# Optimization experiments

Hardware: AMD Instinct MI355X
Metric: run time of the kernel (lower is better)

## Reference

```python
import jax, jax.numpy as jnp
import numpy as np

N_NODES = 50000
N_EDGES = 800000
LN_EPS = 1e-5


def _segment_softmax_aggr(msg, t, dst, n):
    # SoftmaxAggregation(learn=True): alpha = softmax(msg * t) per dest segment, out = sum(alpha * msg)
    logits = msg * t  # [E, C]
    m = jax.ops.segment_max(logits, dst, num_segments=n)
    m = jnp.where(jnp.isfinite(m), m, 0.0)  # empty segments -> 0 to keep exp finite
    e = jnp.exp(logits - m[dst])
    denom = jax.ops.segment_sum(e, dst, num_segments=n)
    alpha = e / jnp.maximum(denom[dst], 1e-16)
    return jax.ops.segment_sum(alpha * msg, dst, num_segments=n)


def _sage_conv(x, src, dst, wp, bp, t, wl, bl, wr):
    # project=True: messages come from relu(lin(x)); root term uses ORIGINAL x
    xp = jax.nn.relu(x @ wp + bp)
    msg = xp[src]                                   # [E, C] gather
    aggr = _segment_softmax_aggr(msg, t, dst, x.shape[0])
    out = aggr @ wl + bl + x @ wr
    # normalize=True: L2 normalize rows (eps as in F.normalize)
    nrm = jnp.maximum(jnp.linalg.norm(out, axis=-1, keepdims=True), 1e-12)
    return out / nrm


def _mem_pool(x, k, w_conv, wl, bl):
    # PyG MemPooling, tau=1: Student-t kernel 1/(1+d^2)
    H, K, F = k.shape
    kk = k.reshape(H * K, F)
    d2 = (jnp.sum(kk * kk, -1)[:, None] + jnp.sum(x * x, -1)[None, :]
          - 2.0 * kk @ x.T)                          # [H*K, N]
    d2 = jnp.maximum(d2, 0.0)
    dist = 1.0 / (1.0 + d2)
    dist = dist.reshape(H, K, -1).transpose(0, 2, 1)  # [H, N, K]
    S = dist / jnp.sum(dist, -1, keepdims=True)       # per-head normalize over clusters
    S = jnp.einsum('h,hnk->nk', w_conv, S)            # 1x1 conv mixing heads (no bias)
    S = jax.nn.softmax(S, axis=-1)                    # [N, K]
    xp = S.T @ x                                      # [K, F]
    return xp @ wl + bl                               # [K, out]


def setup_inputs() -> dict:
    key = jax.random.key(0)
    ks = jax.random.split(key, 20)
    rn = lambda i, shp, s: jax.random.normal(ks[i], shp, dtype=jnp.float32) * s
    inp = {
        'x': rn(0, (N_NODES, 64), 1.0),
        'edge_index': jax.random.randint(ks[1], (2, N_EDGES), 0, N_NODES, dtype=jnp.int32),
        'w_proj1': rn(2, (64, 64), 0.1), 'b_proj1': rn(3, (64,), 0.05),
        't1': jnp.ones((64,), jnp.float32),
        'w_l1': rn(4, (64, 256), 0.1), 'b_l1': rn(5, (256,), 0.05),
        'w_r1': rn(6, (64, 256), 0.1),
        'w_proj2': rn(7, (256, 256), 0.05), 'b_proj2': rn(8, (256,), 0.05),
        't2': jnp.ones((256,), jnp.float32),
        'w_l2': rn(9, (256, 128), 0.05), 'b_l2': rn(10, (128,), 0.05),
        'w_r2': rn(11, (256, 128), 0.05),
        'k_mem': rn(12, (4, 4, 128), 1.0),
        'w_conv': rn(13, (4,), 0.5),
        'w_memlin': rn(14, (128, 128), 0.08), 'b_memlin': rn(15, (128,), 0.05),
        'w_fx': rn(16, (128, 64), 0.08), 'b_fx': rn(17, (64,), 0.05),
        'gamma': jnp.ones((64,), jnp.float32),
        'beta': jnp.zeros((64,), jnp.float32),
    }
    return inp


def reference(x, edge_index, w_proj1, b_proj1, t1, w_l1, b_l1, w_r1,
              w_proj2, b_proj2, t2, w_l2, b_l2, w_r2,
              k_mem, w_conv, w_memlin, b_memlin, w_fx, b_fx, gamma, beta):
    src, dst = edge_index[0], edge_index[1]
    h = _sage_conv(x, src, dst, w_proj1, b_proj1, t1, w_l1, b_l1, w_r1)
    h = jax.nn.relu(h)                              # dropout = identity (eval)
    h = _sage_conv(h, src, dst, w_proj2, b_proj2, t2, w_l2, b_l2, w_r2)
    h = jax.nn.relu(h)
    pooled = _mem_pool(h, k_mem, w_conv, w_memlin, b_memlin)  # [4, 128]
    g = jnp.mean(pooled, axis=0, keepdims=True)     # global_mean_pool -> [1, 128]
    y = g @ w_fx + b_fx                             # [1, 64]
    mu = jnp.mean(y, -1, keepdims=True)
    var = jnp.var(y, -1, keepdims=True)
    y = (y - mu) / jnp.sqrt(var + LN_EPS) * gamma + beta
    return jax.nn.relu(y)
```

## Files before the change

kernel.cpp:

```cpp
#include <hip/hip_runtime.h>
#include <hip/hip_bf16.h>

#define N_NODES 50000
#define N_EDGES 800000
#define NB 196
#define PC_SLICES 2048

typedef __attribute__((ext_vector_type(8))) short short8;
typedef __attribute__((ext_vector_type(4))) float f32x4;
typedef __attribute__((ext_vector_type(2))) float f32x2;

#define QSCALE2 (2.f / 255.f)
#define QINV2   127.5f
#define QSCALE1 (12.75f / 255.f)
#define QINV1   20.f

__device__ __forceinline__ float us2f(unsigned short u) {
    return __uint_as_float(((unsigned int)u) << 16);
}
__device__ __forceinline__ unsigned short f2bu(float f) {
    unsigned int u = __float_as_uint(f);
    unsigned int r = (u + 0x7fffu + ((u >> 16) & 1u)) >> 16;
    return (unsigned short)r;
}
__device__ __forceinline__ float exp2_hw(float x) {
    float r;
    __asm__("v_exp_f32 %0, %1" : "=v"(r) : "v"(x));
    return r;
}
__device__ __forceinline__ void async16(const void* g, void* l) {
    __builtin_amdgcn_global_load_lds(
        (const __attribute__((address_space(1))) unsigned int*)g,
        (__attribute__((address_space(3))) unsigned int*)l, 16, 0, 0);
}
#define LOG2E 1.44269504088896f

__global__ void k_hist(const int* __restrict__ dst, int* __restrict__ counts) {
    int e = blockIdx.x * 256 + threadIdx.x;
    if (e < N_EDGES) atomicAdd(&counts[dst[e]], 1);
}

__global__ __launch_bounds__(256) void k_scan1(const int* __restrict__ counts,
                                               int* __restrict__ row_ptr,
                                               int* __restrict__ partial) {
    __shared__ int sd[256];
    int t = threadIdx.x, i = blockIdx.x * 256 + t;
    int v = (i < N_NODES) ? counts[i] : 0;
    sd[t] = v;
    __syncthreads();
    for (int off = 1; off < 256; off <<= 1) {
        int o = (t >= off) ? sd[t - off] : 0;
        __syncthreads();
        sd[t] += o;
        __syncthreads();
    }
    if (i < N_NODES) row_ptr[i] = sd[t] - v;
    if (t == 255) partial[blockIdx.x] = sd[255];
}

__global__ __launch_bounds__(256) void k_scan3b(int* __restrict__ row_ptr,
                                                const int* __restrict__ partial,
                                                int* __restrict__ cursor) {
    __shared__ int sd[256];
    int t = threadIdx.x;
    sd[t] = (t < blockIdx.x) ? partial[t] : 0;
    __syncthreads();
    for (int off = 128; off > 0; off >>= 1) {
        if (t < off) sd[t] += sd[t + off];
        __syncthreads();
    }
    int base = sd[0];
    int i = blockIdx.x * 256 + t;
    if (i < N_NODES) {
        int v = row_ptr[i] + base;
        row_ptr[i] = v;
        cursor[i] = v;
    }
    if (blockIdx.x == 0 && t == 0) row_ptr[N_NODES] = N_EDGES;
}

__global__ void k_scatter(const int* __restrict__ src, const int* __restrict__ dst,
                          int* __restrict__ cursor, int* __restrict__ src_sorted) {
    int e = blockIdx.x * 256 + threadIdx.x;
    if (e < N_EDGES) {
        int d = dst[e];
        int pos = atomicAdd(&cursor[d], 1);
        src_sorted[pos] = src[e];
    }
}

__global__ __launch_bounds__(256) void k_dhist(const int* __restrict__ counts,
                                               int* __restrict__ bcnt) {
    __shared__ int h[64];
    int t = threadIdx.x;
    if (t < 64) h[t] = 0;
    __syncthreads();
    int i = blockIdx.x * 256 + t;
    if (i < N_NODES) {
        int d = counts[i];
        d = d > 63 ? 63 : d;
        atomicAdd(&h[d], 1);
    }
    __syncthreads();
    if (t < 64) bcnt[blockIdx.x * 64 + t] = h[t];
}

__global__ __launch_bounds__(256) void k_dscan2(const int* __restrict__ bcnt,
                                                int* __restrict__ boff,
                                                int* __restrict__ dtot) {
    __shared__ int sd[256];
    int d = blockIdx.x, t = threadIdx.x;
    int v = (t < NB) ? bcnt[t * 64 + d] : 0;
    sd[t] = v;
    __syncthreads();
    for (int off = 1; off < 256; off <<= 1) {
        int o = (t >= off) ? sd[t - off] : 0;
        __syncthreads();
        sd[t] += o;
        __syncthreads();
    }
    if (t < NB) boff[t * 64 + d] = sd[t] - v;
    if (t == 255) dtot[d] = sd[255];
}

__global__ __launch_bounds__(256) void k_dscatter(const int* __restrict__ counts,
                                                  const int* __restrict__ boff,
                                                  const int* __restrict__ dtot,
                                                  int* __restrict__ perm) {
    __shared__ int h[64];
    __shared__ int dbaseS[64];
    int t = threadIdx.x;
    if (t < 64) {
        h[t] = 0;
        int v = dtot[t];
        int s = v;
        for (int off = 1; off < 64; off <<= 1) {
            int o = __shfl_up(s, off);
            if (t >= off) s += o;
        }
        dbaseS[t] = s - v;
    }
    __syncthreads();
    int i = blockIdx.x * 256 + t;
    if (i < N_NODES) {
        int d = counts[i];
        d = d > 63 ? 63 : d;
        int rank = atomicAdd(&h[d], 1);
        perm[dbaseS[d] + boff[blockIdx.x * 64 + d] + rank] = i;
    }
}

#define XCAST_N (N_NODES * 64)
__global__ __launch_bounds__(256) void k_prep(const float* __restrict__ x,
                                              const float* __restrict__ wp1,
                                              const float* __restrict__ wl1,
                                              const float* __restrict__ wr1,
                                              const float* __restrict__ wp2,
                                              const float* __restrict__ wl2,
                                              const float* __restrict__ wr2,
                                              unsigned short* __restrict__ cat1,
                                              unsigned short* __restrict__ B0T,
                                              unsigned short* __restrict__ B1T,
                                              unsigned short* __restrict__ BP2T,
                                              unsigned short* __restrict__ B2T) {
    int idx = blockIdx.x * 256 + threadIdx.x;
    if (idx < XCAST_N) {
        int i = idx >> 6, j = idx & 63;
        cat1[i * 128 + 64 + j] = f2bu(x[idx]);
        return;
    }
    int w = idx - XCAST_N;
    if (w < 4096)  { int k = w >> 6, n = w & 63;  B0T[n * 64 + k] = f2bu(wp1[w]); return; }
    w -= 4096;
    if (w < 16384) { int k = w >> 8, n = w & 255; B1T[n * 128 + k] = f2bu(wl1[w]); return; }
    w -= 16384;
    if (w < 16384) { int k = w >> 8, n = w & 255; B1T[n * 128 + 64 + k] = f2bu(wr1[w]); return; }
    w -= 16384;
    if (w < 65536) { int k = w >> 8, n = w & 255; BP2T[n * 256 + k] = f2bu(wp2[w]); return; }
    w -= 65536;
    if (w < 32768) { int k = w >> 7, n = w & 127; B2T[n * 512 + k] = f2bu(wl2[w]); return; }
    w -= 32768;
    if (w < 32768) { int k = w >> 7, n = w & 127; B2T[n * 512 + 256 + k] = f2bu(wr2[w]); return; }
}

template<int K, int C, int LDA, int LDOUT, int OUT_OFF, int EP, int WPB, int MH>
__global__ __launch_bounds__(256, WPB) void k_gemm(const unsigned short* __restrict__ A,
                                                   const unsigned short* __restrict__ BT,
                                                   const float* __restrict__ bias,
                                                   void* __restrict__ outv,
                                                   const float* __restrict__ kmem,
                                                   const float* __restrict__ wconv,
                                                   float* __restrict__ Sm,
                                                   float qinv) {
    constexpr int NT = C / 16;
    constexpr int SAE = 64 * MH * 64;
    constexpr int SBE = C * 64;
    constexpr int STAGE_B = (SAE + SBE) * 2;
    constexpr int RPLD = (EP == 2) ? (C + 4) : ((EP == 3) ? (C + 16) : (C + 8));
    constexpr int RP_B = 64 * RPLD * (EP == 2 ? 4 : (EP == 3 ? 1 : 2));
    constexpr int SMEM_B = STAGE_B > RP_B ? STAGE_B : RP_B;
    constexpr int POOL_B = (EP == 2) ? (2048 * 4 + 64 + 16) : 16;
    __shared__ __align__(16) char smem[SMEM_B + POOL_B];
    unsigned short* sA = (unsigned short*)smem;
    unsigned short* sB = sA + SAE;
    float* kls  = (float*)(smem + SMEM_B);
    float* kk2s = kls + 2048;
    float* wcs  = kk2s + 16;

    int t = threadIdx.x;
    int wid = t >> 6, lane = t & 63;
    int lrow = lane & 15, quad = lane >> 4;
    int m0 = blockIdx.x * (64 * MH);

    if (EP == 2) {
        for (int i = t; i < 2048; i += 256) kls[i] = kmem[i];
        if (t < 4) wcs[t] = wconv[t];
        __syncthreads();
        if (t < 16) {
            float s = 0.f;
            for (int f = 0; f < 128; ++f) { float v = kls[t * 128 + f]; s += v * v; }
            kk2s[t] = s;
        }
    }

    f32x4 acc[MH][NT];
#pragma unroll
    for (int h = 0; h < MH; ++h)
#pragma unroll
        for (int nt = 0; nt < NT; ++nt)
#pragma unroll
            for (int r = 0; r < 4; ++r) acc[h][nt][r] = 0.f;

    for (int k0 = 0; k0 < K; k0 += 64) {
        __syncthreads();
        for (int i = t; i < 64 * MH * 8; i += 256) {
            int r = i >> 3, seg = i & 7;
            size_t m = (size_t)(m0 + r);
            async16(&A[m * LDA + k0 + ((seg ^ (r & 7)) << 3)],
                    (char*)sA + (size_t)(i - lane) * 16);
        }
        for (int i = t; i < C * 8; i += 256) {
            int n = i >> 3, seg = i & 7;
            async16(&BT[(size_t)n * K + k0 + ((seg ^ (n & 7)) << 3)],
                    (char*)sB + (size_t)(i - lane) * 16);
        }
        __syncthreads();
#pragma unroll
        for (int kk = 0; kk < 2; ++kk) {
            int sw = lrow & 7;
            short8 av[MH];
#pragma unroll
            for (int h = 0; h < MH; ++h)
                av[h] = *(const short8*)&sA[(h * 64 + wid * 16 + lrow) * 64 +
                                            (((kk * 4 + quad) ^ sw) << 3)];
#pragma unroll
            for (int nt = 0; nt < NT; ++nt) {
                short8 bfg = *(const short8*)&sB[(nt * 16 + lrow) * 64 +
                                                 (((kk * 4 + quad) ^ sw) << 3)];
#pragma unroll
                for (int h = 0; h < MH; ++h)
                    acc[h][nt] = __builtin_amdgcn_mfma_f32_16x16x32_bf16(av[h], bfg, acc[h][nt], 0, 0, 0);
            }
        }
    }

#pragma unroll
    for (int h = 0; h < MH; ++h) {
#pragma unroll
        for (int nt = 0; nt < NT; ++nt) {
            float bv = bias[nt * 16 + lrow];
#pragma unroll
            for (int r = 0; r < 4; ++r) acc[h][nt][r] += bv;
        }
        if (EP == 1 || EP == 2) {
#pragma unroll
            for (int r = 0; r < 4; ++r) {
                float ss = 0.f;
#pragma unroll
                for (int nt = 0; nt < NT; ++nt) ss += acc[h][nt][r] * acc[h][nt][r];
                ss += __shfl_xor(ss, 1);
                ss += __shfl_xor(ss, 2);
                ss += __shfl_xor(ss, 4);
                ss += __shfl_xor(ss, 8);
                float rinv = 1.f / fmaxf(sqrtf(ss), 1e-12f);
#pragma unroll
                for (int nt = 0; nt < NT; ++nt)
                    acc[h][nt][r] = fmaxf(acc[h][nt][r] * rinv, 0.f);
            }
        } else {
#pragma unroll
            for (int nt = 0; nt < NT; ++nt)
#pragma unroll
                for (int r = 0; r < 4; ++r) acc[h][nt][r] = fmaxf(acc[h][nt][r], 0.f);
        }
    }

    __syncthreads();
#pragma unroll
    for (int h = 0; h < MH; ++h) {
        if (EP == 2) {
            float* rp = (float*)smem;
#pragma unroll
            for (int nt = 0; nt < NT; ++nt)
#pragma unroll
                for (int r = 0; r < 4; ++r)
                    rp[(wid * 16 + quad * 4 + r) * RPLD + nt * 16 + lrow] = acc[h][nt][r];
            __syncthreads();
            float* outp = (float*)outv;
            for (int i = t; i < 64 * C / 4; i += 256) {
                int f = i * 4, r = f / C, c = f % C;
                int m = m0 + h * 64 + r;
                if (m < N_NODES)
                    *(float4*)&outp[(size_t)m * LDOUT + OUT_OFF + c] = *(const float4*)&rp[r * RPLD + c];
            }
            {
                int row = t >> 2, p = t & 3;
                int cbase = p * 32;
                float dots[16];
#pragma unroll
                for (int k = 0; k < 16; ++k) dots[k] = 0.f;
                float x2 = 0.f;
#pragma unroll
                for (int j = 0; j < 8; ++j) {
                    int c4 = (j + p * 2) & 7;
                    float4 xv = *(const float4*)&rp[row * RPLD + cbase + c4 * 4];
                    x2 += xv.x * xv.x + xv.y * xv.y + xv.z * xv.z + xv.w * xv.w;
#pragma unroll
                    for (int k = 0; k < 16; ++k) {
                        float4 kv = *(const float4*)&kls[k * 128 + cbase + c4 * 4];
                        dots[k] += xv.x * kv.x + xv.y * kv.y + xv.z * kv.z + xv.w * kv.w;
                    }
                }
#pragma unroll
                for (int k = 0; k < 16; ++k) {
                    dots[k] += __shfl_xor(dots[k], 1);
                    dots[k] += __shfl_xor(dots[k], 2);
                }
                x2 += __shfl_xor(x2, 1);
                x2 += __shfl_xor(x2, 2);
                if (p == 0) {
                    int m = m0 + h * 64 + row;
                    if (m < N_NODES) {
                        float dist[16];
#pragma unroll
                        for (int k = 0; k < 16; ++k) {
                            float d2 = fmaxf(kk2s[k] + x2 - 2.f * dots[k], 0.f);
                            dist[k] = 1.f / (1.f + d2);
                        }
                        float s0 = 0.f, s1 = 0.f, s2 = 0.f, s3 = 0.f;
#pragma unroll
                        for (int hh = 0; hh < 4; ++hh) {
                            float den = dist[hh * 4] + dist[hh * 4 + 1] +
                                        dist[hh * 4 + 2] + dist[hh * 4 + 3];
                            float inv = wcs[hh] / den;
                            s0 += dist[hh * 4 + 0] * inv;
                            s1 += dist[hh * 4 + 1] * inv;
                            s2 += dist[hh * 4 + 2] * inv;
                            s3 += dist[hh * 4 + 3] * inv;
                        }
                        float mx = fmaxf(fmaxf(s0, s1), fmaxf(s2, s3));
                        float e0 = __expf(s0 - mx), e1 = __expf(s1 - mx);
                        float e2 = __expf(s2 - mx), e3 = __expf(s3 - mx);
                        float inv = 1.f / (e0 + e1 + e2 + e3);
                        *(float4*)&Sm[(size_t)m * 4] =
                            make_float4(e0 * inv, e1 * inv, e2 * inv, e3 * inv);
                    }
                }
            }
            __syncthreads();
        } else if (EP == 3) {
            unsigned char* rp = (unsigned char*)smem;
#pragma unroll
            for (int nt = 0; nt < NT; ++nt)
#pragma unroll
                for (int r = 0; r < 4; ++r) {
                    float q = fminf(__builtin_rintf(acc[h][nt][r] * qinv), 255.f);
                    rp[(wid * 16 + quad * 4 + r) * RPLD + nt * 16 + lrow] = (unsigned char)(int)q;
                }
            __syncthreads();
            unsigned char* outp = (unsigned char*)outv;
            for (int i = t; i < 64 * C / 16; i += 256) {
                int f = i * 16, r = f / C, c = f % C;
                int m = m0 + h * 64 + r;
                if (m < N_NODES)
                    *(uint4*)&outp[(size_t)m * LDOUT + OUT_OFF + c] = *(const uint4*)&rp[r * RPLD + c];
            }
            __syncthreads();
        } else {
            unsigned short* rp = (unsigned short*)smem;
#pragma unroll
            for (int nt = 0; nt < NT; ++nt)
#pragma unroll
                for (int r = 0; r < 4; ++r)
                    rp[(wid * 16 + quad * 4 + r) * RPLD + nt * 16 + lrow] = f2bu(acc[h][nt][r]);
            __syncthreads();
            unsigned short* outp = (unsigned short*)outv;
            for (int i = t; i < 64 * C / 8; i += 256) {
                int f = i * 8, r = f / C, c = f % C;
                int m = m0 + h * 64 + r;
                if (m < N_NODES)
                    *(uint4*)&outp[(size_t)m * LDOUT + OUT_OFF + c] = *(const uint4*)&rp[r * RPLD + c];
            }
            __syncthreads();
        }
    }
}

__global__ __launch_bounds__(128) void k_aggr256(const unsigned char* __restrict__ xp,
                                                 const float* __restrict__ tvec,
                                                 const int* __restrict__ row_ptr,
                                                 const int* __restrict__ srcs,
                                                 const int* __restrict__ perm,
                                                 unsigned short* __restrict__ outp) {
    int t = threadIdx.x & 63;
    int wid = threadIdx.x >> 6;
    int n = __builtin_amdgcn_readfirstlane(perm[blockIdx.x * 2 + wid]);
    float4 tv4 = *(const float4*)&tvec[t * 4];
    f32x2 tv01 = {tv4.x * (LOG2E * QSCALE2), tv4.y * (LOG2E * QSCALE2)};
    f32x2 tv23 = {tv4.z * (LOG2E * QSCALE2), tv4.w * (LOG2E * QSCALE2)};
    int beg = __builtin_amdgcn_readfirstlane(row_ptr[n]);
    int end = __builtin_amdgcn_readfirstlane(row_ptr[n + 1]);
    f32x2 se01 = {0.f, 0.f}, se23 = {0.f, 0.f};
    f32x2 sem01 = {0.f, 0.f}, sem23 = {0.f, 0.f};
    int e = beg;
#define EDGE_BODY(VV, MSK)                                                     \
    {                                                                          \
        f32x2 m01 = {(float)((VV) & 0xFFu), (float)(((VV) >> 8) & 0xFFu)};     \
        f32x2 m23 = {(float)(((VV) >> 16) & 0xFFu), (float)((VV) >> 24)};      \
        f32x2 l01 = m01 * tv01, l23 = m23 * tv23;                              \
        f32x2 w01, w23;                                                        \
        w01.x = exp2_hw(l01.x) * (MSK); w01.y = exp2_hw(l01.y) * (MSK);        \
        w23.x = exp2_hw(l23.x) * (MSK); w23.y = exp2_hw(l23.y) * (MSK);        \
        se01 += w01; se23 += w23;                                              \
        sem01 = __builtin_elementwise_fma(w01, m01, sem01);                    \
        sem23 = __builtin_elementwise_fma(w23, m23, sem23);                    \
    }
    for (; e + 16 <= end; e += 16) {
        unsigned int v[16];
#pragma unroll
        for (int j = 0; j < 16; ++j) {
            const unsigned char* p = xp + (size_t)srcs[e + j] * 256;
            v[j] = *(const unsigned int*)&p[t * 4];
        }
#pragma unroll
        for (int j = 0; j < 16; ++j) EDGE_BODY(v[j], 1.f)
    }
    for (; e + 8 <= end; e += 8) {
        unsigned int v[8];
#pragma unroll
        for (int j = 0; j < 8; ++j) {
            const unsigned char* p = xp + (size_t)srcs[e + j] * 256;
            v[j] = *(const unsigned int*)&p[t * 4];
        }
#pragma unroll
        for (int j = 0; j < 8; ++j) EDGE_BODY(v[j], 1.f)
    }
    if (e < end) {
        int last = end - 1;
        unsigned int v[8];
#pragma unroll
        for (int j = 0; j < 8; ++j) {
            int ee = e + j;
            ee = ee < end ? ee : last;
            const unsigned char* p = xp + (size_t)srcs[ee] * 256;
            v[j] = *(const unsigned int*)&p[t * 4];
        }
#pragma unroll
        for (int j = 0; j < 8; ++j) {
            float msk = (e + j < end) ? 1.f : 0.f;
            EDGE_BODY(v[j], msk)
        }
    }
#undef EDGE_BODY
    ushort4 o;
    o.x = f2bu(QSCALE2 * sem01.x / fmaxf(se01.x, 1e-16f));
    o.y = f2bu(QSCALE2 * sem01.y / fmaxf(se01.y, 1e-16f));
    o.z = f2bu(QSCALE2 * sem23.x / fmaxf(se23.x, 1e-16f));
    o.w = f2bu(QSCALE2 * sem23.y / fmaxf(se23.y, 1e-16f));
    *(ushort4*)&outp[(size_t)n * 512 + t * 4] = o;
}

__global__ __launch_bounds__(128) void k_aggr64(const unsigned char* __restrict__ xp,
                                                const float* __restrict__ tvec,
                                                const int* __restrict__ row_ptr,
                                                const int* __restrict__ srcs,
                                                const int* __restrict__ perm,
                                                unsigned short* __restrict__ outp) {
    int c = threadIdx.x & 63;
    int wid = threadIdx.x >> 6;
    int n = __builtin_amdgcn_readfirstlane(perm[blockIdx.x * 2 + wid]);
    float tv = tvec[c] * (LOG2E * QSCALE1);
    int beg = __builtin_amdgcn_readfirstlane(row_ptr[n]);
    int end = __builtin_amdgcn_readfirstlane(row_ptr[n + 1]);
    float se = 0.f, sem = 0.f;
    int e = beg;
    for (; e + 16 <= end; e += 16) {
        unsigned char v[16];
#pragma unroll
        for (int j = 0; j < 16; ++j)
            v[j] = xp[(size_t)srcs[e + j] * 64 + c];
#pragma unroll
        for (int j = 0; j < 16; ++j) {
            float msg = (float)v[j];
            float w = exp2_hw(msg * tv);
            se += w;
            sem = fmaf(w, msg, sem);
        }
    }
    for (; e + 8 <= end; e += 8) {
        unsigned char v[8];
#pragma unroll
        for (int j = 0; j < 8; ++j)
            v[j] = xp[(size_t)srcs[e + j] * 64 + c];
#pragma unroll
        for (int j = 0; j < 8; ++j) {
            float msg = (float)v[j];
            float w = exp2_hw(msg * tv);
            se += w;
            sem = fmaf(w, msg, sem);
        }
    }
    if (e < end) {
        int last = end - 1;
        unsigned char v[8];
#pragma unroll
        for (int j = 0; j < 8; ++j) {
            int ee = e + j;
            ee = ee < end ? ee : last;
            v[j] = xp[(size_t)srcs[ee] * 64 + c];
        }
#pragma unroll
        for (int j = 0; j < 8; ++j) {
            float msk = (e + j < end) ? 1.f : 0.f;
            float msg = (float)v[j];
            float w = exp2_hw(msg * tv) * msk;
            se += w;
            sem = fmaf(w, msg, sem);
        }
    }
    outp[(size_t)n * 128 + c] = f2bu(QSCALE1 * sem / fmaxf(se, 1e-16f));
}

__global__ __launch_bounds__(256) void k_pool_c(const float* __restrict__ h2,
                                                const float* __restrict__ Sm,
                                                float* __restrict__ part) {
    int t = threadIdx.x;
    int c = t & 127, sub = t >> 7;
    int slice = blockIdx.x * 2 + sub;
    float a0 = 0.f, a1 = 0.f, a2 = 0.f, a3 = 0.f;
    for (int n = slice; n < N_NODES; n += PC_SLICES) {
        float xv = h2[(size_t)n * 128 + c];
        float4 sv = *(const float4*)&Sm[(size_t)n * 4];
        a0 = fmaf(sv.x, xv, a0);
        a1 = fmaf(sv.y, xv, a1);
        a2 = fmaf(sv.z, xv, a2);
        a3 = fmaf(sv.w, xv, a3);
    }
    float* p = &part[(size_t)slice * 512];
    p[0 * 128 + c] = a0;
    p[1 * 128 + c] = a1;
    p[2 * 128 + c] = a2;
    p[3 * 128 + c] = a3;
}

__global__ __launch_bounds__(256) void k_pool_b(const float* __restrict__ part,
                                                float* __restrict__ pooled) {
    int j = blockIdx.x;
    float s = 0.f;
    for (int b = threadIdx.x; b < PC_SLICES; b += 256) s += part[(size_t)b * 512 + j];
#pragma unroll
    for (int off = 32; off > 0; off >>= 1) s += __shfl_xor(s, off);
    __shared__ float red[4];
    int lane = threadIdx.x & 63, wid = threadIdx.x >> 6;
    if (lane == 0) red[wid] = s;
    __syncthreads();
    if (threadIdx.x == 0) pooled[j] = red[0] + red[1] + red[2] + red[3];
}

__global__ __launch_bounds__(128) void k_final(const float* __restrict__ pooled,
                                               const float* __restrict__ wmem,
                                               const float* __restrict__ bmem,
                                               const float* __restrict__ wfx,
                                               const float* __restrict__ bfx,
                                               const float* __restrict__ gamma,
                                               const float* __restrict__ beta,
                                               float* __restrict__ out) {
    __shared__ float gx[128], g[128];
    int t = threadIdx.x;
    gx[t] = 0.25f * (pooled[t] + pooled[128 + t] + pooled[256 + t] + pooled[384 + t]);
    __syncthreads();
    float acc = bmem[t];
    for (int f = 0; f < 128; ++f) acc = fmaf(gx[f], wmem[f * 128 + t], acc);
    g[t] = acc;
    __syncthreads();
    if (t < 64) {
        float y = bfx[t];
        for (int f = 0; f < 128; ++f) y = fmaf(g[f], wfx[f * 64 + t], y);
        float s = y, s2 = y * y;
#pragma unroll
        for (int off = 32; off > 0; off >>= 1) {
            s += __shfl_xor(s, off);
            s2 += __shfl_xor(s2, off);
        }
        float mu = s * (1.f / 64.f);
        float var = s2 * (1.f / 64.f) - mu * mu;
        float v = (y - mu) / sqrtf(var + 1e-5f) * gamma[t] + beta[t];
        out[t] = fmaxf(v, 0.f);
    }
}

extern "C" void kernel_launch(void* const* d_in, const int* in_sizes, int n_in,
                              void* d_out, int out_size, void* d_ws, size_t ws_size,
                              hipStream_t stream) {
    const float* x        = (const float*)d_in[0];
    const int*   ei       = (const int*)  d_in[1];
    const float* w_proj1  = (const float*)d_in[2];
    const float* b_proj1  = (const float*)d_in[3];
    const float* t1       = (const float*)d_in[4];
    const float* w_l1     = (const float*)d_in[5];
    const float* b_l1     = (const float*)d_in[6];
    const float* w_r1     = (const float*)d_in[7];
    const float* w_proj2  = (const float*)d_in[8];
    const float* b_proj2  = (const float*)d_in[9];
    const float* t2       = (const float*)d_in[10];
    const float* w_l2     = (const float*)d_in[11];
    const float* b_l2     = (const float*)d_in[12];
    const float* w_r2     = (const float*)d_in[13];
    const float* k_mem    = (const float*)d_in[14];
    const float* w_conv   = (const float*)d_in[15];
    const float* w_memlin = (const float*)d_in[16];
    const float* b_memlin = (const float*)d_in[17];
    const float* w_fx     = (const float*)d_in[18];
    const float* b_fx     = (const float*)d_in[19];
    const float* gamma    = (const float*)d_in[20];
    const float* beta     = (const float*)d_in[21];
    const int* src = ei;
    const int* dst = ei + N_EDGES;
    (void)in_sizes; (void)n_in; (void)out_size; (void)ws_size;

    char* W = (char*)d_ws;
    const size_t MB = 1024 * 1024;
    int*   row_ptr    = (int*)(W + 0);
    int*   cursor     = (int*)(W + 256 * 1024);
    int*   partial    = (int*)(W + 512 * 1024);
    int*   dtot       = (int*)(W + 512 * 1024 + 4096);
    int*   bcnt       = (int*)(W + 520 * 1024);
    int*   boff       = (int*)(W + 576 * 1024);
    int*   src_sorted = (int*)(W + 768 * 1024);
    unsigned short* cat1 = (unsigned short*)(W + 4 * MB);
    unsigned char*  xp1  = (unsigned char*)(W + 17 * MB);
    unsigned short* cat2 = (unsigned short*)(W + 24 * MB);
    unsigned char*  xp2  = (unsigned char*)(W + 76 * MB);
    float* h2     = (float*)(W + 102 * MB);
    float* Sm     = (float*)(W + 128 * MB);
    float* pooled = (float*)(W + 131 * MB);
    unsigned short* B0T  = (unsigned short*)(W + 133 * MB);
    unsigned short* B1T  = (unsigned short*)(W + 134 * MB);
    unsigned short* BP2T = (unsigned short*)(W + 135 * MB);
    unsigned short* B2T  = (unsigned short*)(W + 136 * MB);
    int*   perm   = (int*)(W + 138 * MB);
    float* part   = (float*)(W + 140 * MB);

    hipMemsetAsync(cursor, 0, N_NODES * sizeof(int), stream);
    k_hist<<<(N_EDGES + 255) / 256, 256, 0, stream>>>(dst, cursor);
    k_dhist<<<NB, 256, 0, stream>>>(cursor, bcnt);
    k_scan1<<<NB, 256, 0, stream>>>(cursor, row_ptr, partial);
    k_dscan2<<<64, 256, 0, stream>>>(bcnt, boff, dtot);
    k_dscatter<<<NB, 256, 0, stream>>>(cursor, boff, dtot, perm);
    k_scan3b<<<NB, 256, 0, stream>>>(row_ptr, partial, cursor);
    k_scatter<<<(N_EDGES + 255) / 256, 256, 0, stream>>>(src, dst, cursor, src_sorted);

    k_prep<<<(XCAST_N + 167936 + 255) / 256, 256, 0, stream>>>(
        x, w_proj1, w_l1, w_r1, w_proj2, w_l2, w_r2, cat1, B0T, B1T, BP2T, B2T);

    const int GB = (N_NODES + 127) / 128;
    const int AGB = N_NODES / 2;

    k_gemm<64, 64, 128, 64, 0, 3, 4, 2><<<GB, 256, 0, stream>>>(
        cat1 + 64, B0T, b_proj1, xp1, nullptr, nullptr, nullptr, QINV1);
    k_aggr64<<<AGB, 128, 0, stream>>>(xp1, t1, row_ptr, src_sorted, perm, cat1);
    k_gemm<128, 256, 128, 512, 256, 1, 3, 2><<<GB, 256, 0, stream>>>(
        cat1, B1T, b_l1, cat2, nullptr, nullptr, nullptr, 0.f);

    k_gemm<256, 256, 512, 256, 0, 3, 3, 2><<<GB, 256, 0, stream>>>(
        cat2 + 256, BP2T, b_proj2, xp2, nullptr, nullptr, nullptr, QINV2);
    k_aggr256<<<AGB, 128, 0, stream>>>(xp2, t2, row_ptr, src_sorted, perm, cat2);
    k_gemm<512, 128, 512, 128, 0, 2, 3, 2><<<GB, 256, 0, stream>>>(
        cat2, B2T, b_l2, h2, k_mem, w_conv, Sm, 0.f);

    k_pool_c<<<PC_SLICES / 2, 256, 0, stream>>>(h2, Sm, part);
    k_pool_b<<<512, 256, 0, stream>>>(part, pooled);
    k_final<<<1, 128, 0, stream>>>(pooled, w_memlin, b_memlin, w_fx, b_fx, gamma, beta,
                                   (float*)d_out);
}
```

Baseline: 377.0 us.

## Double-buffer aggregation gathers, reverse degree order, vectorize prep casts

New measurement: 387.0 us. 2.6% more time.

```diff
diff --git a/kernel.cpp b/kernel.cpp
--- a/kernel.cpp
+++ b/kernel.cpp
@@ -151,6 +151,7 @@
 }
 
 #define XCAST_N (N_NODES * 64)
+#define PREP_TOT (XCAST_N + 167936)
 __global__ __launch_bounds__(256) void k_prep(const float* __restrict__ x,
                                               const float* __restrict__ wp1,
                                               const float* __restrict__ wl1,
@@ -163,24 +164,38 @@
                                               unsigned short* __restrict__ B1T,
                                               unsigned short* __restrict__ BP2T,
                                               unsigned short* __restrict__ B2T) {
-    int idx = blockIdx.x * 256 + threadIdx.x;
+    int idx = (blockIdx.x * 256 + threadIdx.x) * 4;
     if (idx < XCAST_N) {
         int i = idx >> 6, j = idx & 63;
-        cat1[i * 128 + 64 + j] = f2bu(x[idx]);
+        float4 v = *(const float4*)&x[idx];
+        ushort4 o = { f2bu(v.x), f2bu(v.y), f2bu(v.z), f2bu(v.w) };
+        *(ushort4*)&cat1[i * 128 + 64 + j] = o;
         return;
     }
     int w = idx - XCAST_N;
-    if (w < 4096)  { int k = w >> 6, n = w & 63;  B0T[n * 64 + k] = f2bu(wp1[w]); return; }
+    if (w < 4096)  { float4 v = *(const float4*)&wp1[w]; int k = w >> 6, n = w & 63;
+                     B0T[n*64+k]=f2bu(v.x); B0T[(n+1)*64+k]=f2bu(v.y);
+                     B0T[(n+2)*64+k]=f2bu(v.z); B0T[(n+3)*64+k]=f2bu(v.w); return; }
     w -= 4096;
-    if (w < 16384) { int k = w >> 8, n = w & 255; B1T[n * 128 + k] = f2bu(wl1[w]); return; }
+    if (w < 16384) { float4 v = *(const float4*)&wl1[w]; int k = w >> 8, n = w & 255;
+                     B1T[n*128+k]=f2bu(v.x); B1T[(n+1)*128+k]=f2bu(v.y);
+                     B1T[(n+2)*128+k]=f2bu(v.z); B1T[(n+3)*128+k]=f2bu(v.w); return; }
     w -= 16384;
-    if (w < 16384) { int k = w >> 8, n = w & 255; B1T[n * 128 + 64 + k] = f2bu(wr1[w]); return; }
+    if (w < 16384) { float4 v = *(const float4*)&wr1[w]; int k = w >> 8, n = w & 255;
+                     B1T[n*128+64+k]=f2bu(v.x); B1T[(n+1)*128+64+k]=f2bu(v.y);
+                     B1T[(n+2)*128+64+k]=f2bu(v.z); B1T[(n+3)*128+64+k]=f2bu(v.w); return; }
     w -= 16384;
-    if (w < 65536) { int k = w >> 8, n = w & 255; BP2T[n * 256 + k] = f2bu(wp2[w]); return; }
+    if (w < 65536) { float4 v = *(const float4*)&wp2[w]; int k = w >> 8, n = w & 255;
+                     BP2T[n*256+k]=f2bu(v.x); BP2T[(n+1)*256+k]=f2bu(v.y);
+                     BP2T[(n+2)*256+k]=f2bu(v.z); BP2T[(n+3)*256+k]=f2bu(v.w); return; }
     w -= 65536;
-    if (w < 32768) { int k = w >> 7, n = w & 127; B2T[n * 512 + k] = f2bu(wl2[w]); return; }
+    if (w < 32768) { float4 v = *(const float4*)&wl2[w]; int k = w >> 7, n = w & 127;
+                     B2T[n*512+k]=f2bu(v.x); B2T[(n+1)*512+k]=f2bu(v.y);
+                     B2T[(n+2)*512+k]=f2bu(v.z); B2T[(n+3)*512+k]=f2bu(v.w); return; }
     w -= 32768;
-    if (w < 32768) { int k = w >> 7, n = w & 127; B2T[n * 512 + 256 + k] = f2bu(wr2[w]); return; }
+    if (w < 32768) { float4 v = *(const float4*)&wr2[w]; int k = w >> 7, n = w & 127;
+                     B2T[n*512+256+k]=f2bu(v.x); B2T[(n+1)*512+256+k]=f2bu(v.y);
+                     B2T[(n+2)*512+256+k]=f2bu(v.z); B2T[(n+3)*512+256+k]=f2bu(v.w); return; }
 }
 
 template<int K, int C, int LDA, int LDOUT, int OUT_OFF, int EP, int WPB, int MH>
@@ -414,7 +429,7 @@
                                                  unsigned short* __restrict__ outp) {
     int t = threadIdx.x & 63;
     int wid = threadIdx.x >> 6;
-    int n = __builtin_amdgcn_readfirstlane(perm[blockIdx.x * 2 + wid]);
+    int n = __builtin_amdgcn_readfirstlane(perm[(N_NODES / 2 - 1 - blockIdx.x) * 2 + wid]);
     float4 tv4 = *(const float4*)&tvec[t * 4];
     f32x2 tv01 = {tv4.x * (LOG2E * QSCALE2), tv4.y * (LOG2E * QSCALE2)};
     f32x2 tv23 = {tv4.z * (LOG2E * QSCALE2), tv4.w * (LOG2E * QSCALE2)};
@@ -422,56 +437,68 @@
     int end = __builtin_amdgcn_readfirstlane(row_ptr[n + 1]);
     f32x2 se01 = {0.f, 0.f}, se23 = {0.f, 0.f};
     f32x2 sem01 = {0.f, 0.f}, sem23 = {0.f, 0.f};
-    int e = beg;
-#define EDGE_BODY(VV, MSK)                                                     \
+
+#define EDGE_BODY(VV)                                                          \
     {                                                                          \
         f32x2 m01 = {(float)((VV) & 0xFFu), (float)(((VV) >> 8) & 0xFFu)};     \
         f32x2 m23 = {(float)(((VV) >> 16) & 0xFFu), (float)((VV) >> 24)};      \
         f32x2 l01 = m01 * tv01, l23 = m23 * tv23;                              \
         f32x2 w01, w23;                                                        \
-        w01.x = exp2_hw(l01.x) * (MSK); w01.y = exp2_hw(l01.y) * (MSK);        \
-        w23.x = exp2_hw(l23.x) * (MSK); w23.y = exp2_hw(l23.y) * (MSK);        \
+        w01.x = exp2_hw(l01.x); w01.y = exp2_hw(l01.y);                        \
+        w23.x = exp2_hw(l23.x); w23.y = exp2_hw(l23.y);                        \
         se01 += w01; se23 += w23;                                              \
         sem01 = __builtin_elementwise_fma(w01, m01, sem01);                    \
         sem23 = __builtin_elementwise_fma(w23, m23, sem23);                    \
     }
-    for (; e + 16 <= end; e += 16) {
-        unsigned int v[16];
-#pragma unroll
-        for (int j = 0; j < 16; ++j) {
-            const unsigned char* p = xp + (size_t)srcs[e + j] * 256;
-            v[j] = *(const unsigned int*)&p[t * 4];
-        }
-#pragma unroll
-        for (int j = 0; j < 16; ++j) EDGE_BODY(v[j], 1.f)
-    }
-    for (; e + 8 <= end; e += 8) {
-        unsigned int v[8];
-#pragma unroll
-        for (int j = 0; j < 8; ++j) {
-            const unsigned char* p = xp + (size_t)srcs[e + j] * 256;
-            v[j] = *(const unsigned int*)&p[t * 4];
-        }
-#pragma unroll
-        for (int j = 0; j < 8; ++j) EDGE_BODY(v[j], 1.f)
-    }
-    if (e < end) {
-        int last = end - 1;
-        unsigned int v[8];
-#pragma unroll
-        for (int j = 0; j < 8; ++j) {
-            int ee = e + j;
-            ee = ee < end ? ee : last;
-            const unsigned char* p = xp + (size_t)srcs[ee] * 256;
-            v[j] = *(const unsigned int*)&p[t * 4];
-        }
-#pragma unroll
-        for (int j = 0; j < 8; ++j) {
-            float msk = (e + j < end) ? 1.f : 0.f;
-            EDGE_BODY(v[j], msk)
+#define LOAD16C(V, E)                                                          \
+    _Pragma("unroll")                                                          \
+    for (int j = 0; j < 16; ++j) {                                             \
+        int ee = (E) + j; ee = ee < end ? ee : end - 1;                        \
+        const unsigned char* p = xp + (size_t)srcs[ee] * 256;                  \
+        V[j] = *(const unsigned int*)&p[t * 4];                                \
+    }
+#define BODY16U(V)                                                             \
+    _Pragma("unroll") for (int j = 0; j < 16; ++j) EDGE_BODY(V[j])
+#define TAIL16(V)                                                              \
+    do {                                                                       \
+        if (end - e == 16) { BODY16U(V) }                                      \
+        else {                                                                 \
+            _Pragma("unroll")                                                  \
+            for (int j = 0; j < 16; ++j) {                                     \
+                unsigned int vv = (e + j < end) ? V[j] : 0u;                   \
+                EDGE_BODY(vv)                                                  \
+            }                                                                  \
+            float ninv = (float)(16 - (end - e));                              \
+            se01.x -= ninv; se01.y -= ninv; se23.x -= ninv; se23.y -= ninv;    \
+        }                                                                      \
+    } while (0)
+
+    unsigned int vA[16], vB[16];
+    int e = beg;
+    int nb = (end - beg + 15) >> 4;
+    if (nb > 0) {
+        LOAD16C(vA, e)
+        int b = 0;
+        while (b + 2 < nb) {
+            LOAD16C(vB, e + 16)
+            BODY16U(vA)
+            LOAD16C(vA, e + 32)
+            BODY16U(vB)
+            e += 32; b += 2;
+        }
+        if (b + 2 == nb) {
+            LOAD16C(vB, e + 16)
+            BODY16U(vA)
+            e += 16;
+            TAIL16(vB);
+        } else {
+            TAIL16(vA);
         }
     }
 #undef EDGE_BODY
+#undef LOAD16C
+#undef BODY16U
+#undef TAIL16
     ushort4 o;
     o.x = f2bu(QSCALE2 * sem01.x / fmaxf(se01.x, 1e-16f));
     o.y = f2bu(QSCALE2 * sem01.y / fmaxf(se01.y, 1e-16f));
@@ -488,56 +515,66 @@
                                                 unsigned short* __restrict__ outp) {
     int c = threadIdx.x & 63;
     int wid = threadIdx.x >> 6;
-    int n = __builtin_amdgcn_readfirstlane(perm[blockIdx.x * 2 + wid]);
+    int n = __builtin_amdgcn_readfirstlane(perm[(N_NODES / 2 - 1 - blockIdx.x) * 2 + wid]);
     float tv = tvec[c] * (LOG2E * QSCALE1);
     int beg = __builtin_amdgcn_readfirstlane(row_ptr[n]);
     int end = __builtin_amdgcn_readfirstlane(row_ptr[n + 1]);
     float se = 0.f, sem = 0.f;
+
+#define EDGE_BODY1(VV)                                                         \
+    {                                                                          \
+        float msg = (float)(VV);                                               \
+        float w = exp2_hw(msg * tv);                                           \
+        se += w;                                                               \
+        sem = fmaf(w, msg, sem);                                               \
+    }
+#define LOAD16C1(V, E)                                                         \
+    _Pragma("unroll")                                                          \
+    for (int j = 0; j < 16; ++j) {                                             \
+        int ee = (E) + j; ee = ee < end ? ee : end - 1;                        \
+        V[j] = xp[(size_t)srcs[ee] * 64 + c];                                  \
+    }
+#define BODY16U1(V)                                                            \
+    _Pragma("unroll") for (int j = 0; j < 16; ++j) EDGE_BODY1(V[j])
+#define TAIL161(V)                                                             \
+    do {                                                                       \
+        if (end - e == 16) { BODY16U1(V) }                                     \
+        else {                                                                 \
+            _Pragma("unroll")                                                  \
+            for (int j = 0; j < 16; ++j) {                                     \
+                unsigned int vv = (e + j < end) ? (unsigned int)V[j] : 0u;     \
+                EDGE_BODY1(vv)                                                 \
+            }                                                                  \
+            se -= (float)(16 - (end - e));                                     \
+        }                                                                      \
+    } while (0)
+
+    unsigned char vA[16], vB[16];
     int e = beg;
-    for (; e + 16 <= end; e += 16) {
-        unsigned char v[16];
-#pragma unroll
-        for (int j = 0; j < 16; ++j)
-            v[j] = xp[(size_t)srcs[e + j] * 64 + c];
-#pragma unroll
-        for (int j = 0; j < 16; ++j) {
-            float msg = (float)v[j];
-            float w = exp2_hw(msg * tv);
-            se += w;
-            sem = fmaf(w, msg, sem);
-        }
-    }
-    for (; e + 8 <= end; e += 8) {
-        unsigned char v[8];
-#pragma unroll
-        for (int j = 0; j < 8; ++j)
-            v[j] = xp[(size_t)srcs[e + j] * 64 + c];
-#pragma unroll
-        for (int j = 0; j < 8; ++j) {
-            float msg = (float)v[j];
-            float w = exp2_hw(msg * tv);
-            se += w;
-            sem = fmaf(w, msg, sem);
-        }
-    }
-    if (e < end) {
-        int last = end - 1;
-        unsigned char v[8];
-#pragma unroll
-        for (int j = 0; j < 8; ++j) {
-            int ee = e + j;
-            ee = ee < end ? ee : last;
-            v[j] = xp[(size_t)srcs[ee] * 64 + c];
-        }
-#pragma unroll
-        for (int j = 0; j < 8; ++j) {
-            float msk = (e + j < end) ? 1.f : 0.f;
-            float msg = (float)v[j];
-            float w = exp2_hw(msg * tv) * msk;
-            se += w;
-            sem = fmaf(w, msg, sem);
-        }
-    }
+    int nb = (end - beg + 15) >> 4;
+    if (nb > 0) {
+        LOAD16C1(vA, e)
+        int b = 0;
+        while (b + 2 < nb) {
+            LOAD16C1(vB, e + 16)
+            BODY16U1(vA)
+            LOAD16C1(vA, e + 32)
+            BODY16U1(vB)
+            e += 32; b += 2;
+        }
+        if (b + 2 == nb) {
+            LOAD16C1(vB, e + 16)
+            BODY16U1(vA)
+            e += 16;
+            TAIL161(vB);
+        } else {
+            TAIL161(vA);
+        }
+    }
+#undef EDGE_BODY1
+#undef LOAD16C1
+#undef BODY16U1
+#undef TAIL161
     outp[(size_t)n * 128 + c] = f2bu(QSCALE1 * sem / fmaxf(se, 1e-16f));
 }
 
@@ -670,7 +707,7 @@
     k_scan3b<<<NB, 256, 0, stream>>>(row_ptr, partial, cursor);
     k_scatter<<<(N_EDGES + 255) / 256, 256, 0, stream>>>(src, dst, cursor, src_sorted);
 
-    k_prep<<<(XCAST_N + 167936 + 255) / 256, 256, 0, stream>>>(
+    k_prep<<<(PREP_TOT / 4 + 255) / 256, 256, 0, stream>>>(
         x, w_proj1, w_l1, w_r1, w_proj2, w_l2, w_r2, cat1, B0T, B1T, BP2T, B2T);
 
     const int GB = (N_NODES + 127) / 128;
```

## Use persistent grid-stride aggregation kernels and vectorize the prep cast

Applied to the files above, without the earlier changes.

Measured after the change: 374.0 us. Within noise of the previous version (-0.8%).

```diff
diff --git a/kernel.cpp b/kernel.cpp
--- a/kernel.cpp
+++ b/kernel.cpp
@@ -5,6 +5,7 @@
 #define N_EDGES 800000
 #define NB 196
 #define PC_SLICES 2048
+#define AGG_GRID 2048
 
 typedef __attribute__((ext_vector_type(8))) short short8;
 typedef __attribute__((ext_vector_type(4))) float f32x4;
@@ -151,6 +152,7 @@
 }
 
 #define XCAST_N (N_NODES * 64)
+#define PREP_TOT (XCAST_N + 167936)
 __global__ __launch_bounds__(256) void k_prep(const float* __restrict__ x,
                                               const float* __restrict__ wp1,
                                               const float* __restrict__ wl1,
@@ -163,24 +165,38 @@
                                               unsigned short* __restrict__ B1T,
                                               unsigned short* __restrict__ BP2T,
                                               unsigned short* __restrict__ B2T) {
-    int idx = blockIdx.x * 256 + threadIdx.x;
+    int idx = (blockIdx.x * 256 + threadIdx.x) * 4;
     if (idx < XCAST_N) {
         int i = idx >> 6, j = idx & 63;
-        cat1[i * 128 + 64 + j] = f2bu(x[idx]);
+        float4 v = *(const float4*)&x[idx];
+        ushort4 o = { f2bu(v.x), f2bu(v.y), f2bu(v.z), f2bu(v.w) };
+        *(ushort4*)&cat1[i * 128 + 64 + j] = o;
         return;
     }
     int w = idx - XCAST_N;
-    if (w < 4096)  { int k = w >> 6, n = w & 63;  B0T[n * 64 + k] = f2bu(wp1[w]); return; }
+    if (w < 4096)  { float4 v = *(const float4*)&wp1[w]; int k = w >> 6, n = w & 63;
+                     B0T[n*64+k]=f2bu(v.x); B0T[(n+1)*64+k]=f2bu(v.y);
+                     B0T[(n+2)*64+k]=f2bu(v.z); B0T[(n+3)*64+k]=f2bu(v.w); return; }
     w -= 4096;
-    if (w < 16384) { int k = w >> 8, n = w & 255; B1T[n * 128 + k] = f2bu(wl1[w]); return; }
+    if (w < 16384) { float4 v = *(const float4*)&wl1[w]; int k = w >> 8, n = w & 255;
+                     B1T[n*128+k]=f2bu(v.x); B1T[(n+1)*128+k]=f2bu(v.y);
+                     B1T[(n+2)*128+k]=f2bu(v.z); B1T[(n+3)*128+k]=f2bu(v.w); return; }
     w -= 16384;
-    if (w < 16384) { int k = w >> 8, n = w & 255; B1T[n * 128 + 64 + k] = f2bu(wr1[w]); return; }
+    if (w < 16384) { float4 v = *(const float4*)&wr1[w]; int k = w >> 8, n = w & 255;
+                     B1T[n*128+64+k]=f2bu(v.x); B1T[(n+1)*128+64+k]=f2bu(v.y);
+                     B1T[(n+2)*128+64+k]=f2bu(v.z); B1T[(n+3)*128+64+k]=f2bu(v.w); return; }
     w -= 16384;
-    if (w < 65536) { int k = w >> 8, n = w & 255; BP2T[n * 256 + k] = f2bu(wp2[w]); return; }
+    if (w < 65536) { float4 v = *(const float4*)&wp2[w]; int k = w >> 8, n = w & 255;
+                     BP2T[n*256+k]=f2bu(v.x); BP2T[(n+1)*256+k]=f2bu(v.y);
+                     BP2T[(n+2)*256+k]=f2bu(v.z); BP2T[(n+3)*256+k]=f2bu(v.w); return; }
     w -= 65536;
-    if (w < 32768) { int k = w >> 7, n = w & 127; B2T[n * 512 + k] = f2bu(wl2[w]); return; }
+    if (w < 32768) { float4 v = *(const float4*)&wl2[w]; int k = w >> 7, n = w & 127;
+                     B2T[n*512+k]=f2bu(v.x); B2T[(n+1)*512+k]=f2bu(v.y);
+                     B2T[(n+2)*512+k]=f2bu(v.z); B2T[(n+3)*512+k]=f2bu(v.w); return; }
     w -= 32768;
-    if (w < 32768) { int k = w >> 7, n = w & 127; B2T[n * 512 + 256 + k] = f2bu(wr2[w]); return; }
+    if (w < 32768) { float4 v = *(const float4*)&wr2[w]; int k = w >> 7, n = w & 127;
+                     B2T[n*512+256+k]=f2bu(v.x); B2T[(n+1)*512+256+k]=f2bu(v.y);
+                     B2T[(n+2)*512+256+k]=f2bu(v.z); B2T[(n+3)*512+256+k]=f2bu(v.w); return; }
 }
 
 template<int K, int C, int LDA, int LDOUT, int OUT_OFF, int EP, int WPB, int MH>
@@ -406,23 +422,17 @@
     }
 }
 
-__global__ __launch_bounds__(128) void k_aggr256(const unsigned char* __restrict__ xp,
-                                                 const float* __restrict__ tvec,
-                                                 const int* __restrict__ row_ptr,
-                                                 const int* __restrict__ srcs,
-                                                 const int* __restrict__ perm,
-                                                 unsigned short* __restrict__ outp) {
+__global__ __launch_bounds__(256, 8) void k_aggr256(const unsigned char* __restrict__ xp,
+                                                    const float* __restrict__ tvec,
+                                                    const int* __restrict__ row_ptr,
+                                                    const int* __restrict__ srcs,
+                                                    const int* __restrict__ perm,
+                                                    unsigned short* __restrict__ outp) {
     int t = threadIdx.x & 63;
     int wid = threadIdx.x >> 6;
-    int n = __builtin_amdgcn_readfirstlane(perm[blockIdx.x * 2 + wid]);
     float4 tv4 = *(const float4*)&tvec[t * 4];
     f32x2 tv01 = {tv4.x * (LOG2E * QSCALE2), tv4.y * (LOG2E * QSCALE2)};
     f32x2 tv23 = {tv4.z * (LOG2E * QSCALE2), tv4.w * (LOG2E * QSCALE2)};
-    int beg = __builtin_amdgcn_readfirstlane(row_ptr[n]);
-    int end = __builtin_amdgcn_readfirstlane(row_ptr[n + 1]);
-    f32x2 se01 = {0.f, 0.f}, se23 = {0.f, 0.f};
-    f32x2 sem01 = {0.f, 0.f}, sem23 = {0.f, 0.f};
-    int e = beg;
 #define EDGE_BODY(VV, MSK)                                                     \
     {                                                                          \
         f32x2 m01 = {(float)((VV) & 0xFFu), (float)(((VV) >> 8) & 0xFFu)};     \
@@ -435,110 +445,122 @@
         sem01 = __builtin_elementwise_fma(w01, m01, sem01);                    \
         sem23 = __builtin_elementwise_fma(w23, m23, sem23);                    \
     }
-    for (; e + 16 <= end; e += 16) {
-        unsigned int v[16];
-#pragma unroll
-        for (int j = 0; j < 16; ++j) {
-            const unsigned char* p = xp + (size_t)srcs[e + j] * 256;
-            v[j] = *(const unsigned int*)&p[t * 4];
-        }
-#pragma unroll
-        for (int j = 0; j < 16; ++j) EDGE_BODY(v[j], 1.f)
-    }
-    for (; e + 8 <= end; e += 8) {
-        unsigned int v[8];
-#pragma unroll
-        for (int j = 0; j < 8; ++j) {
-            const unsigned char* p = xp + (size_t)srcs[e + j] * 256;
-            v[j] = *(const unsigned int*)&p[t * 4];
-        }
-#pragma unroll
-        for (int j = 0; j < 8; ++j) EDGE_BODY(v[j], 1.f)
-    }
-    if (e < end) {
-        int last = end - 1;
-        unsigned int v[8];
-#pragma unroll
-        for (int j = 0; j < 8; ++j) {
-            int ee = e + j;
-            ee = ee < end ? ee : last;
-            const unsigned char* p = xp + (size_t)srcs[ee] * 256;
-            v[j] = *(const unsigned int*)&p[t * 4];
-        }
-#pragma unroll
-        for (int j = 0; j < 8; ++j) {
-            float msk = (e + j < end) ? 1.f : 0.f;
-            EDGE_BODY(v[j], msk)
-        }
+    for (int g = blockIdx.x; g < N_NODES / 4; g += AGG_GRID) {
+        int grp = N_NODES / 4 - 1 - g;
+        int n = __builtin_amdgcn_readfirstlane(perm[grp * 4 + wid]);
+        int beg = __builtin_amdgcn_readfirstlane(row_ptr[n]);
+        int end = __builtin_amdgcn_readfirstlane(row_ptr[n + 1]);
+        f32x2 se01 = {0.f, 0.f}, se23 = {0.f, 0.f};
+        f32x2 sem01 = {0.f, 0.f}, sem23 = {0.f, 0.f};
+        int e = beg;
+        for (; e + 16 <= end; e += 16) {
+            unsigned int v[16];
+#pragma unroll
+            for (int j = 0; j < 16; ++j) {
+                const unsigned char* p = xp + (size_t)srcs[e + j] * 256;
+                v[j] = *(const unsigned int*)&p[t * 4];
+            }
+#pragma unroll
+            for (int j = 0; j < 16; ++j) EDGE_BODY(v[j], 1.f)
+        }
+        for (; e + 8 <= end; e += 8) {
+            unsigned int v[8];
+#pragma unroll
+            for (int j = 0; j < 8; ++j) {
+                const unsigned char* p = xp + (size_t)srcs[e + j] * 256;
+                v[j] = *(const unsigned int*)&p[t * 4];
+            }
+#pragma unroll
+            for (int j = 0; j < 8; ++j) EDGE_BODY(v[j], 1.f)
+        }
+        if (e < end) {
+            int last = end - 1;
+            unsigned int v[8];
+#pragma unroll
+            for (int j = 0; j < 8; ++j) {
+                int ee = e + j;
+                ee = ee < end ? ee : last;
+                const unsigned char* p = xp + (size_t)srcs[ee] * 256;
+                v[j] = *(const unsigned int*)&p[t * 4];
+            }
+#pragma unroll
+            for (int j = 0; j < 8; ++j) {
+                float msk = (e + j < end) ? 1.f : 0.f;
+                EDGE_BODY(v[j], msk)
+            }
+        }
+        ushort4 o;
+        o.x = f2bu(QSCALE2 * sem01.x / fmaxf(se01.x, 1e-16f));
+        o.y = f2bu(QSCALE2 * sem01.y / fmaxf(se01.y, 1e-16f));
+        o.z = f2bu(QSCALE2 * sem23.x / fmaxf(se23.x, 1e-16f));
+        o.w = f2bu(QSCALE2 * sem23.y / fmaxf(se23.y, 1e-16f));
+        *(ushort4*)&outp[(size_t)n * 512 + t * 4] = o;
     }
 #undef EDGE_BODY
-    ushort4 o;
-    o.x = f2bu(QSCALE2 * sem01.x / fmaxf(se01.x, 1e-16f));
-    o.y = f2bu(QSCALE2 * sem01.y / fmaxf(se01.y, 1e-16f));
-    o.z = f2bu(QSCALE2 * sem23.x / fmaxf(se23.x, 1e-16f));
-    o.w = f2bu(QSCALE2 * sem23.y / fmaxf(se23.y, 1e-16f));
-    *(ushort4*)&outp[(size_t)n * 512 + t * 4] = o;
-}
-
-__global__ __launch_bounds__(128) void k_aggr64(const unsigned char* __restrict__ xp,
-                                                const float* __restrict__ tvec,
-                                                const int* __restrict__ row_ptr,
-                                                const int* __restrict__ srcs,
-                                                const int* __restrict__ perm,
-                                                unsigned short* __restrict__ outp) {
+}
+
+__global__ __launch_bounds__(256, 8) void k_aggr64(const unsigned char* __restrict__ xp,
+                                                   const float* __restrict__ tvec,
+                                                   const int* __restrict__ row_ptr,
+                                                   const int* __restrict__ srcs,
+                                                   const int* __restrict__ perm,
+                                                   unsigned short* __restrict__ outp) {
     int c = threadIdx.x & 63;
     int wid = threadIdx.x >> 6;
-    int n = __builtin_amdgcn_readfirstlane(perm[blockIdx.x * 2 + wid]);
     float tv = tvec[c] * (LOG2E * QSCALE1);
-    int beg = __builtin_amdgcn_readfirstlane(row_ptr[n]);
-    int end = __builtin_amdgcn_readfirstlane(row_ptr[n + 1]);
-    float se = 0.f, sem = 0.f;
-    int e = beg;
-    for (; e + 16 <= end; e += 16) {
-        unsigned char v[16];
-#pragma unroll
-        for (int j = 0; j < 16; ++j)
-            v[j] = xp[(size_t)srcs[e + j] * 64 + c];
-#pragma unroll
-        for (int j = 0; j < 16; ++j) {
-            float msg = (float)v[j];
-            float w = exp2_hw(msg * tv);
-            se += w;
-            sem = fmaf(w, msg, sem);
-        }
-    }
-    for (; e + 8 <= end; e += 8) {
-        unsigned char v[8];
-#pragma unroll
-        for (int j = 0; j < 8; ++j)
-            v[j] = xp[(size_t)srcs[e + j] * 64 + c];
-#pragma unroll
-        for (int j = 0; j < 8; ++j) {
-            float msg = (float)v[j];
-            float w = exp2_hw(msg * tv);
-            se += w;
-            sem = fmaf(w, msg, sem);
-        }
-    }
-    if (e < end) {
-        int last = end - 1;
-        unsigned char v[8];
-#pragma unroll
-        for (int j = 0; j < 8; ++j) {
-            int ee = e + j;
-            ee = ee < end ? ee : last;
-            v[j] = xp[(size_t)srcs[ee] * 64 + c];
-        }
-#pragma unroll
-        for (int j = 0; j < 8; ++j) {
-            float msk = (e + j < end) ? 1.f : 0.f;
-            float msg = (float)v[j];
-            float w = exp2_hw(msg * tv) * msk;
-            se += w;
-            sem = fmaf(w, msg, sem);
-        }
-    }
-    outp[(size_t)n * 128 + c] = f2bu(QSCALE1 * sem / fmaxf(se, 1e-16f));
+    for (int g = blockIdx.x; g < N_NODES / 4; g += AGG_GRID) {
+        int grp = N_NODES / 4 - 1 - g;
+        int n = __builtin_amdgcn_readfirstlane(perm[grp * 4 + wid]);
+        int beg = __builtin_amdgcn_readfirstlane(row_ptr[n]);
+        int end = __builtin_amdgcn_readfirstlane(row_ptr[n + 1]);
+        float se = 0.f, sem = 0.f;
+        int e = beg;
+        for (; e + 16 <= end; e += 16) {
+            unsigned char v[16];
+#pragma unroll
+            for (int j = 0; j < 16; ++j)
+                v[j] = xp[(size_t)srcs[e + j] * 64 + c];
+#pragma unroll
+            for (int j = 0; j < 16; ++j) {
+                float msg = (float)v[j];
+                float w = exp2_hw(msg * tv);
+                se += w;
+                sem = fmaf(w, msg, sem);
+            }
+        }
+        for (; e + 8 <= end; e += 8) {
+            unsigned char v[8];
+#pragma unroll
+            for (int j = 0; j < 8; ++j)
+                v[j] = xp[(size_t)srcs[e + j] * 64 + c];
+#pragma unroll
+            for (int j = 0; j < 8; ++j) {
+                float msg = (float)v[j];
+                float w = exp2_hw(msg * tv);
+                se += w;
+                sem = fmaf(w, msg, sem);
+            }
+        }
+        if (e < end) {
+            int last = end - 1;
+            unsigned char v[8];
+#pragma unroll
+            for (int j = 0; j < 8; ++j) {
+                int ee = e + j;
+                ee = ee < end ? ee : last;
+                v[j] = xp[(size_t)srcs[ee] * 64 + c];
+            }
+#pragma unroll
+            for (int j = 0; j < 8; ++j) {
+                float msk = (e + j < end) ? 1.f : 0.f;
+                float msg = (float)v[j];
+                float w = exp2_hw(msg * tv) * msk;
+                se += w;
+                sem = fmaf(w, msg, sem);
+            }
+        }
+        outp[(size_t)n * 128 + c] = f2bu(QSCALE1 * sem / fmaxf(se, 1e-16f));
+    }
 }
 
 __global__ __launch_bounds__(256) void k_pool_c(const float* __restrict__ h2,
@@ -670,21 +692,20 @@
     k_scan3b<<<NB, 256, 0, stream>>>(row_ptr, partial, cursor);
     k_scatter<<<(N_EDGES + 255) / 256, 256, 0, stream>>>(src, dst, cursor, src_sorted);
 
-    k_prep<<<(XCAST_N + 167936 + 255) / 256, 256, 0, stream>>>(
+    k_prep<<<(PREP_TOT / 4 + 255) / 256, 256, 0, stream>>>(
         x, w_proj1, w_l1, w_r1, w_proj2, w_l2, w_r2, cat1, B0T, B1T, BP2T, B2T);
 
     const int GB = (N_NODES + 127) / 128;
-    const int AGB = N_NODES / 2;
 
     k_gemm<64, 64, 128, 64, 0, 3, 4, 2><<<GB, 256, 0, stream>>>(
         cat1 + 64, B0T, b_proj1, xp1, nullptr, nullptr, nullptr, QINV1);
-    k_aggr64<<<AGB, 128, 0, stream>>>(xp1, t1, row_ptr, src_sorted, perm, cat1);
+    k_aggr64<<<AGG_GRID, 256, 0, stream>>>(xp1, t1, row_ptr, src_sorted, perm, cat1);
     k_gemm<128, 256, 128, 512, 256, 1, 3, 2><<<GB, 256, 0, stream>>>(
         cat1, B1T, b_l1, cat2, nullptr, nullptr, nullptr, 0.f);
 
     k_gemm<256, 256, 512, 256, 0, 3, 3, 2><<<GB, 256, 0, stream>>>(
         cat2 + 256, BP2T, b_proj2, xp2, nullptr, nullptr, nullptr, QINV2);
-    k_aggr256<<<AGB, 128, 0, stream>>>(xp2, t2, row_ptr, src_sorted, perm, cat2);
+    k_aggr256<<<AGG_GRID, 256, 0, stream>>>(xp2, t2, row_ptr, src_sorted, perm, cat2);
     k_gemm<512, 128, 512, 128, 0, 2, 3, 2><<<GB, 256, 0, stream>>>(
         cat2, B2T, b_l2, h2, k_mem, w_conv, Sm, 0.f);
 
```
